# Performance work log

Measured on AMD Instinct MI355X. Metric: run time of the kernel, lower is better.

Reference implementation:

```python
import jax, jax.numpy as jnp
import numpy as np

NBIT = 8
QMAX = 2 ** (NBIT - 1) - 1  # 127, symmetric 8-bit range


def _sym_scale(x):
    # symmetric_linear_quantization_params: scale = max|x| / (2^(b-1)-1)
    return jnp.max(jnp.abs(x)) / QMAX


def setup_inputs() -> dict:
    key = jax.random.key(0)
    k1, k2, k3 = jax.random.split(key, 3)
    B, DIN, DOUT = 8192, 2048, 8192
    x = jax.random.normal(k1, (B, DIN), jnp.float32)
    weight = jax.random.normal(k2, (DOUT, DIN), jnp.float32) * 0.02
    bias = jax.random.normal(k3, (DOUT,), jnp.float32) * 0.01
    return {"x": x, "weight": weight, "bias": bias}


def reference(x, weight, bias):
    # --- QuantAct 1: symmetric 8-bit activation quantization ---
    s_a = _sym_scale(x)                                   # scalar act scale
    x_int = jnp.clip(jnp.round(x / s_a), -QMAX, QMAX)     # int8 values in fp32
    # --- QuantLinear: per-output-channel 8-bit weight quant + integer GEMM ---
    s_w = jnp.max(jnp.abs(weight), axis=1) / QMAX         # [DOUT] weight scales
    w_int = jnp.clip(jnp.round(weight / s_w[:, None]), -QMAX, QMAX)
    s_b = s_w * s_a                                        # output/bias scale [DOUT]
    b_int = jnp.round(bias / s_b)
    out_int = x_int @ w_int.T + b_int                      # [B, DOUT] int accumulation
    out = out_int * s_b                                    # dequantize
    # --- QuantAct 2: requantize output, symmetric 8-bit ---
    s_o = _sym_scale(out)
    out_q = jnp.clip(jnp.round(out / s_o), -QMAX, QMAX) * s_o
    return out_q
```

## Files before the change

kernel.cpp:

```cpp
#include <hip/hip_runtime.h>
#include <stdint.h>

#define B_DIM 8192
#define DIN   2048
#define DOUT  8192
#define NKT   (DIN / 128)

typedef int  v4i __attribute__((ext_vector_type(4)));
typedef char c8  __attribute__((ext_vector_type(8)));

__device__ __forceinline__ void gload_lds16(const void* g, void* l) {
  __builtin_amdgcn_global_load_lds(
      (const __attribute__((address_space(1))) void*)g,
      (__attribute__((address_space(3))) void*)l, 16, 0, 0);
}

__device__ __forceinline__ float wave_max(float m) {
#pragma unroll
  for (int off = 32; off; off >>= 1) m = fmaxf(m, __shfl_xor(m, off, 64));
  return m;
}

__global__ void k_init(unsigned int* p) {
  p[0] = 0u;
  p[1] = 0u;
}

__global__ __launch_bounds__(256) void k_absmax(const float4* __restrict__ x,
                                                int n4,
                                                unsigned int* __restrict__ out_bits) {
  int idx = blockIdx.x * blockDim.x + threadIdx.x;
  int stride = gridDim.x * blockDim.x;
  float m = 0.f;
  for (int i = idx; i < n4; i += stride) {
    float4 v = x[i];
    m = fmaxf(m, fabsf(v.x));
    m = fmaxf(m, fabsf(v.y));
    m = fmaxf(m, fabsf(v.z));
    m = fmaxf(m, fabsf(v.w));
  }
  m = wave_max(m);
  __shared__ float red[4];
  if ((threadIdx.x & 63) == 0) red[threadIdx.x >> 6] = m;
  __syncthreads();
  if (threadIdx.x == 0) {
    m = fmaxf(fmaxf(red[0], red[1]), fmaxf(red[2], red[3]));
    atomicMax(out_bits, __float_as_uint(m));
  }
}

__global__ void k_quant_x(const float* __restrict__ x, c8* __restrict__ xq,
                          int n8, const unsigned int* __restrict__ sa_bits) {
  int i = blockIdx.x * blockDim.x + threadIdx.x;
  if (i >= n8) return;
  float s_a = __uint_as_float(*sa_bits) / 127.0f;
  const float4* p = (const float4*)(x + (size_t)i * 8);
  float4 v0 = p[0], v1 = p[1];
  float vv[8] = {v0.x, v0.y, v0.z, v0.w, v1.x, v1.y, v1.z, v1.w};
  c8 q;
#pragma unroll
  for (int j = 0; j < 8; ++j) {
    float r = fminf(fmaxf(rintf(vv[j] / s_a), -127.f), 127.f);
    q[j] = (char)(int)r;
  }
  xq[i] = q;
}

__global__ __launch_bounds__(256) void k_quant_w(const float* __restrict__ w,
                                                 c8* __restrict__ wq,
                                                 float* __restrict__ s_w) {
  int row = blockIdx.x;
  int tid = threadIdx.x;
  const float4* wr = (const float4*)(w + (size_t)row * DIN);
  float4 v0 = wr[tid * 2], v1 = wr[tid * 2 + 1];
  float vv[8] = {v0.x, v0.y, v0.z, v0.w, v1.x, v1.y, v1.z, v1.w};
  float m = 0.f;
#pragma unroll
  for (int j = 0; j < 8; ++j) m = fmaxf(m, fabsf(vv[j]));
  m = wave_max(m);
  __shared__ float wmax[4];
  if ((tid & 63) == 0) wmax[tid >> 6] = m;
  __syncthreads();
  m = fmaxf(fmaxf(wmax[0], wmax[1]), fmaxf(wmax[2], wmax[3]));
  float s = m / 127.0f;
  if (tid == 0) s_w[row] = s;
  c8 q;
#pragma unroll
  for (int j = 0; j < 8; ++j) {
    float r = fminf(fmaxf(rintf(vv[j] / s), -127.f), 127.f);
    q[j] = (char)(int)r;
  }
  wq[(size_t)row * (DIN / 8) + tid] = q;
}

__global__ __launch_bounds__(512, 2) void k_gemm8(
    const char* __restrict__ Aq, const char* __restrict__ Bq,
    const float* __restrict__ s_w, const float* __restrict__ bias,
    const unsigned int* __restrict__ sa_bits, float* __restrict__ out,
    unsigned int* __restrict__ omax_bits) {
  __shared__ __align__(16) char lds[131072];

  const int tid = threadIdx.x;
  const int lane = tid & 63;
  const int wave = tid >> 6;
  const int wm = wave >> 2;
  const int wn = wave & 3;

  const int orig = blockIdx.x;
  const int xcd = orig & 7;
  const int k = orig >> 3;
  const int bx = (xcd & 3) * 8 + (k & 7);
  const int by = (xcd >> 2) * 16 + (k >> 3);
  const int row0 = by * 256, col0 = bx * 256;

  const int srow = ((tid >> 6) << 4) | (tid & 15);
  const int skb = tid & 48;
  const char* aS = Aq + (size_t)(row0 + srow) * DIN + skb;
  const char* bS = Bq + (size_t)(col0 + srow) * DIN + skb;

  auto STAGE = [&](int kt, int ks) {
    if (kt >= NKT) kt -= 2;
    int slot = kt & 1;
    const char* srcA = aS + (size_t)kt * 128 + ks * 64;
    const char* srcB = bS + (size_t)kt * 128 + ks * 64;
    int dstA = slot * 65536 + ks * 16384 + tid * 16;
    gload_lds16(srcA, &lds[dstA]);
    gload_lds16(srcA + (size_t)128 * DIN, &lds[dstA + 8192]);
    gload_lds16(srcB, &lds[dstA + 32768]);
    gload_lds16(srcB + (size_t)128 * DIN, &lds[dstA + 40960]);
  };

  v4i acc[2][4][4];
#pragma unroll
  for (int mh = 0; mh < 2; ++mh)
#pragma unroll
    for (int mf = 0; mf < 4; ++mf)
#pragma unroll
      for (int nf = 0; nf < 4; ++nf) acc[mh][mf][nf] = (v4i){0, 0, 0, 0};

  const int lb = lane * 16;

#define PHASE(SLOT, KS, SKT, SKS)                                            \
  do {                                                                       \
    const int abase = (SLOT) * 65536 + (KS) * 16384;                         \
    v4i b_[4], a_[4];                                                        \
    _Pragma("unroll") for (int nf = 0; nf < 4; ++nf) b_[nf] =                \
        *(const v4i*)&lds[abase + 32768 + (wn * 4 + nf) * 1024 + lb];        \
    _Pragma("unroll") for (int mf = 0; mf < 4; ++mf) a_[mf] =                \
        *(const v4i*)&lds[abase + (wm * 8 + mf) * 1024 + lb];                \
    asm volatile("s_waitcnt vmcnt(4)" ::: "memory");                         \
    asm volatile("s_barrier" ::: "memory");                                  \
    STAGE(SKT, SKS);                                                         \
    __builtin_amdgcn_s_setprio(1);                                           \
    _Pragma("unroll") for (int mf = 0; mf < 4; ++mf)                         \
        _Pragma("unroll") for (int nf = 0; nf < 4; ++nf) acc[0][mf][nf] =    \
        __builtin_amdgcn_mfma_i32_16x16x64_i8(a_[mf], b_[nf],                \
                                              acc[0][mf][nf], 0, 0, 0);      \
    __builtin_amdgcn_s_setprio(0);                                           \
    _Pragma("unroll") for (int mf = 0; mf < 4; ++mf) a_[mf] =                \
        *(const v4i*)&lds[abase + (wm * 8 + 4 + mf) * 1024 + lb];            \
    __builtin_amdgcn_s_setprio(1);                                           \
    _Pragma("unroll") for (int mf = 0; mf < 4; ++mf)                         \
        _Pragma("unroll") for (int nf = 0; nf < 4; ++nf) acc[1][mf][nf] =    \
        __builtin_amdgcn_mfma_i32_16x16x64_i8(a_[mf], b_[nf],                \
                                              acc[1][mf][nf], 0, 0, 0);      \
    __builtin_amdgcn_s_setprio(0);                                           \
  } while (0)

  STAGE(0, 0);
  STAGE(0, 1);
  STAGE(1, 0);
  asm volatile("s_waitcnt vmcnt(4)" ::: "memory");
  asm volatile("s_barrier" ::: "memory");

#pragma unroll 1
  for (int i = 0; i < NKT / 2; ++i) {
    const int t0 = 2 * i, t1 = 2 * i + 1;
    PHASE(0, 0, t0 + 1, 1);
    PHASE(0, 1, t0 + 2, 0);
    PHASE(1, 0, t1 + 1, 1);
    PHASE(1, 1, t1 + 2, 0);
  }
#undef PHASE

  const int fr = lane & 15;
  float s_a = __uint_as_float(*sa_bits) / 127.0f;
  float lmax = 0.f;
#pragma unroll
  for (int nf = 0; nf < 4; ++nf) {
    int col = col0 + wn * 64 + nf * 16 + fr;
    float sw = s_w[col];
    float sb = sw * s_a;
    float bint = rintf(bias[col] / sb);
#pragma unroll
    for (int mh = 0; mh < 2; ++mh)
#pragma unroll
      for (int mf = 0; mf < 4; ++mf) {
        int rbase = row0 + wm * 128 + mh * 64 + mf * 16 + (lane >> 4) * 4;
#pragma unroll
        for (int r = 0; r < 4; ++r) {
          float o = ((float)acc[mh][mf][nf][r] + bint) * sb;
          out[(size_t)(rbase + r) * DOUT + col] = o;
          lmax = fmaxf(lmax, fabsf(o));
        }
      }
  }
  lmax = wave_max(lmax);
  asm volatile("s_waitcnt vmcnt(0)" ::: "memory");
  __syncthreads();
  float* red = (float*)lds;
  if (lane == 0) red[wave] = lmax;
  __syncthreads();
  if (tid == 0) {
    float m = 0.f;
#pragma unroll
    for (int w2 = 0; w2 < 8; ++w2) m = fmaxf(m, red[w2]);
    atomicMax(omax_bits, __float_as_uint(m));
  }
}

__global__ void k_requant(float4* __restrict__ out, int n4,
                          const unsigned int* __restrict__ omax_bits) {
  float s_o = __uint_as_float(*omax_bits) / 127.0f;
  int idx = blockIdx.x * blockDim.x + threadIdx.x;
  int stride = gridDim.x * blockDim.x;
  for (int i = idx; i < n4; i += stride) {
    float4 v = out[i];
    v.x = fminf(fmaxf(rintf(v.x / s_o), -127.f), 127.f) * s_o;
    v.y = fminf(fmaxf(rintf(v.y / s_o), -127.f), 127.f) * s_o;
    v.z = fminf(fmaxf(rintf(v.z / s_o), -127.f), 127.f) * s_o;
    v.w = fminf(fmaxf(rintf(v.w / s_o), -127.f), 127.f) * s_o;
    out[i] = v;
  }
}

extern "C" void kernel_launch(void* const* d_in, const int* in_sizes, int n_in,
                              void* d_out, int out_size, void* d_ws,
                              size_t ws_size, hipStream_t stream) {
  const float* x = (const float*)d_in[0];
  const float* w = (const float*)d_in[1];
  const float* bias = (const float*)d_in[2];
  float* out = (float*)d_out;
  char* ws = (char*)d_ws;

  unsigned int* absbits = (unsigned int*)ws;
  float* s_w = (float*)(ws + 512);
  char* xq = ws + 65536;
  char* wq = ws + 65536 + (size_t)B_DIM * DIN;

  k_init<<<1, 1, 0, stream>>>(absbits);
  k_absmax<<<1024, 256, 0, stream>>>((const float4*)x, B_DIM * DIN / 4, absbits);
  k_quant_x<<<(B_DIM * DIN / 8) / 256, 256, 0, stream>>>(x, (c8*)xq,
                                                         B_DIM * DIN / 8, absbits);
  k_quant_w<<<DOUT, 256, 0, stream>>>(w, (c8*)wq, s_w);
  k_gemm8<<<1024, 512, 0, stream>>>(xq, wq, s_w, bias, absbits, out, absbits + 1);
  k_requant<<<4096, 256, 0, stream>>>((float4*)out, B_DIM * DOUT / 4, absbits + 1);
}
```

Baseline: 350.3 us.

## Double-buffer LDS fragment loads in registers across K phases

Restructures the int8 MFMA main loop so each phase prefetches the next phase's B fragments and first-half A fragments into a second register set right after the barrier. The MFMAs then consume fragments already in registers, overlapping LDS read latency with matrix math. The prologue now waits only for the first stage and preloads the initial fragments. This costs about 32 extra VGPRs, which could reduce occupancy or cause spills, and it changes the ordering between barriers and LDS reads.

```diff
diff --git a/kernel.cpp b/kernel.cpp
--- a/kernel.cpp
+++ b/kernel.cpp
@@ -139,47 +139,52 @@
       for (int nf = 0; nf < 4; ++nf) acc[mh][mf][nf] = (v4i){0, 0, 0, 0};
 
   const int lb = lane * 16;
-
-#define PHASE(SLOT, KS, SKT, SKS)                                            \
-  do {                                                                       \
-    const int abase = (SLOT) * 65536 + (KS) * 16384;                         \
-    v4i b_[4], a_[4];                                                        \
-    _Pragma("unroll") for (int nf = 0; nf < 4; ++nf) b_[nf] =                \
-        *(const v4i*)&lds[abase + 32768 + (wn * 4 + nf) * 1024 + lb];        \
-    _Pragma("unroll") for (int mf = 0; mf < 4; ++mf) a_[mf] =                \
-        *(const v4i*)&lds[abase + (wm * 8 + mf) * 1024 + lb];                \
-    asm volatile("s_waitcnt vmcnt(4)" ::: "memory");                         \
-    asm volatile("s_barrier" ::: "memory");                                  \
-    STAGE(SKT, SKS);                                                         \
-    __builtin_amdgcn_s_setprio(1);                                           \
-    _Pragma("unroll") for (int mf = 0; mf < 4; ++mf)                         \
-        _Pragma("unroll") for (int nf = 0; nf < 4; ++nf) acc[0][mf][nf] =    \
-        __builtin_amdgcn_mfma_i32_16x16x64_i8(a_[mf], b_[nf],                \
-                                              acc[0][mf][nf], 0, 0, 0);      \
-    __builtin_amdgcn_s_setprio(0);                                           \
-    _Pragma("unroll") for (int mf = 0; mf < 4; ++mf) a_[mf] =                \
-        *(const v4i*)&lds[abase + (wm * 8 + 4 + mf) * 1024 + lb];            \
-    __builtin_amdgcn_s_setprio(1);                                           \
-    _Pragma("unroll") for (int mf = 0; mf < 4; ++mf)                         \
-        _Pragma("unroll") for (int nf = 0; nf < 4; ++nf) acc[1][mf][nf] =    \
-        __builtin_amdgcn_mfma_i32_16x16x64_i8(a_[mf], b_[nf],                \
-                                              acc[1][mf][nf], 0, 0, 0);      \
-    __builtin_amdgcn_s_setprio(0);                                           \
+  v4i b0[4], al0[4], b1[4], al1[4];
+
+#define PHASE(CSLOT, CKS, CUR_B, CUR_AL, NSLOT, NKS, NXT_B, NXT_AL, SKT, SKS) \
+  do {                                                                        \
+    asm volatile("s_waitcnt vmcnt(4)" ::: "memory");                          \
+    asm volatile("s_barrier" ::: "memory");                                   \
+    STAGE(SKT, SKS);                                                          \
+    const int nb = (NSLOT)*65536 + (NKS)*16384;                               \
+    _Pragma("unroll") for (int nf = 0; nf < 4; ++nf) NXT_B[nf] =              \
+        *(const v4i*)&lds[nb + 32768 + (wn * 4 + nf) * 1024 + lb];            \
+    _Pragma("unroll") for (int mf = 0; mf < 4; ++mf) NXT_AL[mf] =             \
+        *(const v4i*)&lds[nb + (wm * 8 + mf) * 1024 + lb];                    \
+    const int cb = (CSLOT)*65536 + (CKS)*16384;                               \
+    v4i ah[4];                                                                \
+    _Pragma("unroll") for (int mf = 0; mf < 4; ++mf) ah[mf] =                 \
+        *(const v4i*)&lds[cb + (wm * 8 + 4 + mf) * 1024 + lb];                \
+    __builtin_amdgcn_s_setprio(1);                                            \
+    _Pragma("unroll") for (int mf = 0; mf < 4; ++mf)                          \
+        _Pragma("unroll") for (int nf = 0; nf < 4; ++nf) acc[0][mf][nf] =     \
+        __builtin_amdgcn_mfma_i32_16x16x64_i8(CUR_AL[mf], CUR_B[nf],          \
+                                              acc[0][mf][nf], 0, 0, 0);       \
+    _Pragma("unroll") for (int mf = 0; mf < 4; ++mf)                          \
+        _Pragma("unroll") for (int nf = 0; nf < 4; ++nf) acc[1][mf][nf] =     \
+        __builtin_amdgcn_mfma_i32_16x16x64_i8(ah[mf], CUR_B[nf],              \
+                                              acc[1][mf][nf], 0, 0, 0);       \
+    __builtin_amdgcn_s_setprio(0);                                            \
   } while (0)
 
   STAGE(0, 0);
   STAGE(0, 1);
   STAGE(1, 0);
-  asm volatile("s_waitcnt vmcnt(4)" ::: "memory");
+  asm volatile("s_waitcnt vmcnt(8)" ::: "memory");
   asm volatile("s_barrier" ::: "memory");
+#pragma unroll
+  for (int nf = 0; nf < 4; ++nf)
+    b0[nf] = *(const v4i*)&lds[32768 + (wn * 4 + nf) * 1024 + lb];
+#pragma unroll
+  for (int mf = 0; mf < 4; ++mf)
+    al0[mf] = *(const v4i*)&lds[(wm * 8 + mf) * 1024 + lb];
 
 #pragma unroll 1
   for (int i = 0; i < NKT / 2; ++i) {
-    const int t0 = 2 * i, t1 = 2 * i + 1;
-    PHASE(0, 0, t0 + 1, 1);
-    PHASE(0, 1, t0 + 2, 0);
-    PHASE(1, 0, t1 + 1, 1);
-    PHASE(1, 1, t1 + 2, 0);
+    PHASE(0, 0, b0, al0, 0, 1, b1, al1, 2 * i + 1, 1);
+    PHASE(0, 1, b1, al1, 1, 0, b0, al0, 2 * i + 2, 0);
+    PHASE(1, 0, b0, al0, 1, 1, b1, al1, 2 * i + 2, 1);
+    PHASE(1, 1, b1, al1, 0, 0, b0, al0, 2 * i + 3, 0);
   }
 #undef PHASE
 
```

Measured after the change: 345.6 us. About the same (-1.4%).

## Split GEMM main loop into finer half-phases with separate A/B staging

Applied to the files above, without the earlier changes.

Restructures the int8 MFMA main loop so each phase computes one M-half and issues a single A- or B-operand global-to-LDS stage, doubling the number of phases per K tile. The vmcnt wait now happens only every fourth phase, and explicit lgkmcnt waits, sched_barrier and a second s_barrier bracket the MFMA block. The aim is to spread global loads more evenly across compute and so overlap memory with MFMA better. In exchange it adds more barriers per iteration and depends on the new prefetch ordering and wait counts being correct.

```diff
diff --git a/kernel.cpp b/kernel.cpp
--- a/kernel.cpp
+++ b/kernel.cpp
@@ -118,16 +118,13 @@
   const char* aS = Aq + (size_t)(row0 + srow) * DIN + skb;
   const char* bS = Bq + (size_t)(col0 + srow) * DIN + skb;
 
-  auto STAGE = [&](int kt, int ks) {
+  auto STAGE = [&](int kt, int isB, int ks) {
     if (kt >= NKT) kt -= 2;
-    int slot = kt & 1;
-    const char* srcA = aS + (size_t)kt * 128 + ks * 64;
-    const char* srcB = bS + (size_t)kt * 128 + ks * 64;
-    int dstA = slot * 65536 + ks * 16384 + tid * 16;
-    gload_lds16(srcA, &lds[dstA]);
-    gload_lds16(srcA + (size_t)128 * DIN, &lds[dstA + 8192]);
-    gload_lds16(srcB, &lds[dstA + 32768]);
-    gload_lds16(srcB + (size_t)128 * DIN, &lds[dstA + 40960]);
+    const int slot = kt & 1;
+    const char* src = (isB ? bS : aS) + (size_t)kt * 128 + ks * 64;
+    const int dst = slot * 65536 + isB * 32768 + ks * 16384 + tid * 16;
+    gload_lds16(src, &lds[dst]);
+    gload_lds16(src + (size_t)128 * DIN, &lds[dst + 8192]);
   };
 
   v4i acc[2][4][4];
@@ -139,49 +136,58 @@
       for (int nf = 0; nf < 4; ++nf) acc[mh][mf][nf] = (v4i){0, 0, 0, 0};
 
   const int lb = lane * 16;
-
-#define PHASE(SLOT, KS, SKT, SKS)                                            \
+  v4i b_[4];
+
+#define PH(SLOT, KS, MH, SKT, SISB, SKS, WAITV)                              \
   do {                                                                       \
-    const int abase = (SLOT) * 65536 + (KS) * 16384;                         \
-    v4i b_[4], a_[4];                                                        \
-    _Pragma("unroll") for (int nf = 0; nf < 4; ++nf) b_[nf] =                \
-        *(const v4i*)&lds[abase + 32768 + (wn * 4 + nf) * 1024 + lb];        \
+    v4i a_[4];                                                               \
+    const int ab =                                                           \
+        (SLOT) * 65536 + (KS) * 16384 + (wm * 8 + (MH) * 4) * 1024 + lb;     \
     _Pragma("unroll") for (int mf = 0; mf < 4; ++mf) a_[mf] =                \
-        *(const v4i*)&lds[abase + (wm * 8 + mf) * 1024 + lb];                \
-    asm volatile("s_waitcnt vmcnt(4)" ::: "memory");                         \
+        *(const v4i*)&lds[ab + mf * 1024];                                   \
+    if (!(MH)) {                                                             \
+      const int bb =                                                         \
+          (SLOT) * 65536 + 32768 + (KS) * 16384 + (wn * 4) * 1024 + lb;      \
+      _Pragma("unroll") for (int nf = 0; nf < 4; ++nf) b_[nf] =              \
+          *(const v4i*)&lds[bb + nf * 1024];                                 \
+    }                                                                        \
+    STAGE(SKT, SISB, SKS);                                                   \
+    if (WAITV) asm volatile("s_waitcnt vmcnt(6)" ::: "memory");              \
     asm volatile("s_barrier" ::: "memory");                                  \
-    STAGE(SKT, SKS);                                                         \
+    asm volatile("s_waitcnt lgkmcnt(0)" ::: "memory");                       \
+    __builtin_amdgcn_sched_barrier(0);                                       \
     __builtin_amdgcn_s_setprio(1);                                           \
     _Pragma("unroll") for (int mf = 0; mf < 4; ++mf)                         \
-        _Pragma("unroll") for (int nf = 0; nf < 4; ++nf) acc[0][mf][nf] =    \
+        _Pragma("unroll") for (int nf = 0; nf < 4; ++nf) acc[MH][mf][nf] =   \
         __builtin_amdgcn_mfma_i32_16x16x64_i8(a_[mf], b_[nf],                \
-                                              acc[0][mf][nf], 0, 0, 0);      \
+                                              acc[MH][mf][nf], 0, 0, 0);     \
     __builtin_amdgcn_s_setprio(0);                                           \
-    _Pragma("unroll") for (int mf = 0; mf < 4; ++mf) a_[mf] =                \
-        *(const v4i*)&lds[abase + (wm * 8 + 4 + mf) * 1024 + lb];            \
-    __builtin_amdgcn_s_setprio(1);                                           \
-    _Pragma("unroll") for (int mf = 0; mf < 4; ++mf)                         \
-        _Pragma("unroll") for (int nf = 0; nf < 4; ++nf) acc[1][mf][nf] =    \
-        __builtin_amdgcn_mfma_i32_16x16x64_i8(a_[mf], b_[nf],                \
-                                              acc[1][mf][nf], 0, 0, 0);      \
-    __builtin_amdgcn_s_setprio(0);                                           \
+    asm volatile("s_barrier" ::: "memory");                                  \
   } while (0)
 
-  STAGE(0, 0);
-  STAGE(0, 1);
-  STAGE(1, 0);
-  asm volatile("s_waitcnt vmcnt(4)" ::: "memory");
+  STAGE(0, 1, 0);
+  STAGE(0, 0, 0);
+  STAGE(0, 1, 1);
+  STAGE(0, 0, 1);
+  STAGE(1, 1, 0);
+  STAGE(1, 0, 0);
+  STAGE(1, 1, 1);
+  asm volatile("s_waitcnt vmcnt(6)" ::: "memory");
   asm volatile("s_barrier" ::: "memory");
 
 #pragma unroll 1
   for (int i = 0; i < NKT / 2; ++i) {
-    const int t0 = 2 * i, t1 = 2 * i + 1;
-    PHASE(0, 0, t0 + 1, 1);
-    PHASE(0, 1, t0 + 2, 0);
-    PHASE(1, 0, t1 + 1, 1);
-    PHASE(1, 1, t1 + 2, 0);
-  }
-#undef PHASE
+    const int t1 = 2 * i + 1, t2 = 2 * i + 2, t3 = 2 * i + 3;
+    PH(0, 0, 0, t1, 0, 1, false);
+    PH(0, 0, 1, t2, 1, 0, false);
+    PH(0, 1, 0, t2, 0, 0, false);
+    PH(0, 1, 1, t2, 1, 1, true);
+    PH(1, 0, 0, t2, 0, 1, false);
+    PH(1, 0, 1, t3, 1, 0, false);
+    PH(1, 1, 0, t3, 0, 0, false);
+    PH(1, 1, 1, t3, 1, 1, true);
+  }
+#undef PH
 
   const int fr = lane & 15;
   float s_a = __uint_as_float(*sa_bits) / 127.0f;
```

Result: no change. 345.6 us (-1.4%).
